# Kernel optimization log

Measured on AMD Instinct MI355X. Metric: run time of the kernel, lower is better.

The kernel has to match this reference:

```python
import jax, jax.numpy as jnp
import numpy as np

H = 8      # head count
ES = 96    # per-head dim
EMB = H * ES
L = 6      # layers
B, T = 8, 512
LN_EPS = 1e-5

def _layernorm(x, g, b):
    mu = jnp.mean(x, axis=-1, keepdims=True)
    var = jnp.mean(jnp.square(x - mu), axis=-1, keepdims=True)
    return (x - mu) * jax.lax.rsqrt(var + LN_EPS) * g + b

def setup_inputs() -> dict:
    key = jax.random.key(0)
    ks = jax.random.split(key, 6)
    s = 0.02
    return {
        "x": jax.random.normal(ks[0], (B, T, EMB), jnp.float32),
        "Wkqv": jax.random.normal(ks[1], (L, 3 * ES, ES), jnp.float32) * s,
        "Wproj": jax.random.normal(ks[2], (L, EMB, EMB), jnp.float32) * s,
        "ln1_g": jnp.ones((L, EMB), jnp.float32),
        "ln1_b": jnp.zeros((L, EMB), jnp.float32),
        "ln2_g": jnp.ones((L, EMB), jnp.float32),
        "ln2_b": jnp.zeros((L, EMB), jnp.float32),
        "ff_w1": jax.random.normal(ks[3], (L, 4 * EMB, EMB), jnp.float32) * s,
        "ff_b1": jnp.zeros((L, 4 * EMB), jnp.float32),
        "ff_w2": jax.random.normal(ks[4], (L, EMB, 4 * EMB), jnp.float32) * s,
        "ff_b2": jnp.zeros((L, EMB), jnp.float32),
    }

def _forward(x, Wkqv, Wproj, ln1_g, ln1_b, ln2_g, ln2_b, ff_w1, ff_b1, ff_w2, ff_b2):
    scale = 1.0 / jnp.sqrt(jnp.float32(ES))

    def step(carry, p):
        x, prev = carry
        wkqv, wproj, g1, b1, g2, b2, w1, bb1, w2, bb2 = p
        Bx, Tx, _ = x.shape
        xh = x.reshape(Bx, Tx, H, ES)                         # [B,T,H,es]
        kqv = jnp.einsum('bthe,fe->bthf', xh, wkqv)           # [B,T,H,3es]
        k, q, v = jnp.split(kqv, 3, axis=-1)                  # torch.split order: k,q,v
        # residual attention: raw scores + previous layer's raw scores
        score = jnp.einsum('bihk,bjhk->bijh', q, k) * scale + prev  # [B,T,T,H]
        att = jax.nn.softmax(score, axis=2)                   # over key axis j
        res = jnp.einsum('btih,bihs->bths', att, v).reshape(Bx, Tx, EMB)
        res = res @ wproj.T
        x = _layernorm(x + res, g1, b1)
        ff = jax.nn.gelu(x @ w1.T + bb1, approximate=False) @ w2.T + bb2
        x = _layernorm(x + ff, g2, b2)
        return (x, score), None

    prev0 = jnp.zeros((x.shape[0], x.shape[1], x.shape[1], H), x.dtype)
    (x, _), _ = jax.lax.scan(step, (x, prev0),
                             (Wkqv, Wproj, ln1_g, ln1_b, ln2_g, ln2_b,
                              ff_w1, ff_b1, ff_w2, ff_b2))
    return x

def reference(x, Wkqv, Wproj, ln1_g, ln1_b, ln2_g, ln2_b, ff_w1, ff_b1, ff_w2, ff_b2):
    return _forward(x, Wkqv, Wproj, ln1_g, ln1_b, ln2_g, ln2_b, ff_w1, ff_b1, ff_w2, ff_b2)
```

## Files before the change

### kernel.cpp

```cpp
#include <hip/hip_runtime.h>
#include <math.h>

#define BB 8
#define TT 512
#define HH 8
#define ESS 96
#define EMBD 768
#define FFD 3072
#define NLAYER 6
#define KHMAX 576

typedef unsigned short ushort_t;
typedef __attribute__((ext_vector_type(8))) short short8;
typedef __attribute__((ext_vector_type(4))) float f32x4;
typedef __attribute__((ext_vector_type(4))) unsigned short ushort4v;
typedef __attribute__((ext_vector_type(8))) unsigned short ushort8v;

static __device__ __forceinline__ ushort_t f2b(float f) {
    unsigned u = __builtin_bit_cast(unsigned, f);
    unsigned r = (u + 0x7fffu + ((u >> 16) & 1u)) >> 16;
    return (ushort_t)r;
}
static __device__ __forceinline__ float b2f(ushort_t u) {
    return __builtin_bit_cast(float, ((unsigned)u) << 16);
}

#define GLDS(gp, lp) __builtin_amdgcn_global_load_lds( \
    (const __attribute__((address_space(1))) void*)(gp), \
    (__attribute__((address_space(3))) void*)(lp), 16, 0, 0)

template<int BM, int BN, int WM, int WN, int OUTBF, int HASBIAS, int GELU, int BETA>
__global__ __launch_bounds__(256) void gemm_mfma(
    const ushort_t* __restrict__ A, int lda,
    const ushort_t* __restrict__ B, int ldb,
    void* __restrict__ Cv, int ldc,
    int K, float alpha,
    const float* __restrict__ bias,
    int bdiv, long sAb, long sAh, long sBb, long sBh, long sCb, long sCh)
{
    constexpr int BK = 32;
    constexpr int WTM = BM / WM;
    constexpr int WTN = BN / WN;
    constexpr int MF = WTM / 16, NF = WTN / 16;
    constexpr int ACH = (BM * BK * 2) / 1024;
    constexpr int BCH = (BN * BK * 2) / 1024;

    const int z = blockIdx.z;
    const int zb = z / bdiv, zh = z % bdiv;
    A += (long)zb * sAb + (long)zh * sAh;
    B += (long)zb * sBb + (long)zh * sBh;
    const long coff = (long)zb * sCb + (long)zh * sCh;

    __shared__ ushort_t As[BM * BK];
    __shared__ ushort_t Bs[BN * BK];

    const int tid = threadIdx.x;
    const int w = tid >> 6, lane = tid & 63;
    const int wr = w / WN, wc = w % WN;
    const int m0 = blockIdx.y * BM;
    const int n0 = blockIdx.x * BN;

    f32x4 acc[MF][NF] = {};

    const int fr = lane & 15;
    const int kb = lane >> 4;
    const int swz = ((fr >> 1) & 3) << 3;
    const int rl = lane >> 2;
    const int cl = ((lane & 3) * 8) ^ (((rl >> 1) & 3) << 3);

    for (int k0 = 0; k0 < K; k0 += BK) {
#pragma unroll
        for (int q = 0; q < (ACH + 3) / 4; ++q) {
            int ci = q * 4 + w;
            if (ci < ACH) {
                int r = ci * 16 + rl;
                GLDS(A + (long)(m0 + r) * lda + (k0 + cl), (char*)As + ci * 1024);
            }
        }
#pragma unroll
        for (int q = 0; q < (BCH + 3) / 4; ++q) {
            int ci = q * 4 + w;
            if (ci < BCH) {
                int r = ci * 16 + rl;
                GLDS(B + (long)(n0 + r) * ldb + (k0 + cl), (char*)Bs + ci * 1024);
            }
        }
        __syncthreads();

        short8 af[MF], bfr[NF];
#pragma unroll
        for (int fm = 0; fm < MF; ++fm)
            af[fm] = *(const short8*)&As[(wr * WTM + fm * 16 + fr) * 32 + (kb * 8 ^ swz)];
#pragma unroll
        for (int fn = 0; fn < NF; ++fn)
            bfr[fn] = *(const short8*)&Bs[(wc * WTN + fn * 16 + fr) * 32 + (kb * 8 ^ swz)];
#pragma unroll
        for (int fm = 0; fm < MF; ++fm)
#pragma unroll
            for (int fn = 0; fn < NF; ++fn)
                acc[fm][fn] = __builtin_amdgcn_mfma_f32_16x16x32_bf16(
                    af[fm], bfr[fn], acc[fm][fn], 0, 0, 0);
        __syncthreads();
    }

    const int cr = lane >> 4;
    const int cc = lane & 15;
#pragma unroll
    for (int fm = 0; fm < MF; ++fm) {
#pragma unroll
        for (int fn = 0; fn < NF; ++fn) {
#pragma unroll
            for (int j = 0; j < 4; ++j) {
                int gm = m0 + wr * WTM + fm * 16 + cr * 4 + j;
                int gn = n0 + wc * WTN + fn * 16 + cc;
                float v = alpha * acc[fm][fn][j];
                if (HASBIAS) v += bias[gn];
                if (GELU) {
                    float zz = 1.5957691216f * fmaf(0.044715f * v * v, v, v);
                    v = v / (1.f + __expf(-zz));
                }
                long idx = coff + (long)gm * ldc + gn;
                if (BETA) v += ((const float*)Cv)[idx];
                if (OUTBF) ((ushort_t*)Cv)[idx] = f2b(v);
                else       ((float*)Cv)[idx] = v;
            }
        }
    }
}

__global__ __launch_bounds__(256) void kqv_gemm(
    const ushort_t* __restrict__ A,
    const ushort_t* __restrict__ Bw,
    ushort_t* __restrict__ Kh, ushort_t* __restrict__ Qh,
    ushort_t* __restrict__ Vt, int loff, float scale)
{
    constexpr int BM = 128, BN = 96, BK = 32;
    __shared__ ushort_t As[BM * BK];
    __shared__ ushort_t Bs[BN * BK];

    const int tid = threadIdx.x;
    const int w = tid >> 6, lane = tid & 63;
    const int m0 = blockIdx.y * BM;
    const int n0 = blockIdx.x * BN;

    f32x4 acc[2][6] = {};
    const int fr = lane & 15;
    const int kb = lane >> 4;
    const int swz = ((fr >> 1) & 3) << 3;
    const int rl = lane >> 2;
    const int cl = ((lane & 3) * 8) ^ (((rl >> 1) & 3) << 3);

    for (int k0 = 0; k0 < 96; k0 += BK) {
#pragma unroll
        for (int q = 0; q < 2; ++q) {
            int ci = q * 4 + w;
            int r = ci * 16 + rl;
            GLDS(A + (long)(m0 + r) * ESS + (k0 + cl), (char*)As + ci * 1024);
        }
        {
            int ci = w;
            int r = ci * 16 + rl;
            GLDS(Bw + (long)(n0 + r) * ESS + (k0 + cl), (char*)Bs + ci * 1024);
            if (w < 2) {
                int ci2 = 4 + w;
                int r2 = ci2 * 16 + rl;
                GLDS(Bw + (long)(n0 + r2) * ESS + (k0 + cl), (char*)Bs + ci2 * 1024);
            }
        }
        __syncthreads();

        short8 af[2], bfr[6];
#pragma unroll
        for (int fm = 0; fm < 2; ++fm)
            af[fm] = *(const short8*)&As[(w * 32 + fm * 16 + fr) * 32 + (kb * 8 ^ swz)];
#pragma unroll
        for (int fn = 0; fn < 6; ++fn)
            bfr[fn] = *(const short8*)&Bs[(fn * 16 + fr) * 32 + (kb * 8 ^ swz)];
#pragma unroll
        for (int fm = 0; fm < 2; ++fm)
#pragma unroll
            for (int fn = 0; fn < 6; ++fn)
                acc[fm][fn] = __builtin_amdgcn_mfma_f32_16x16x32_bf16(
                    af[fm], bfr[fn], acc[fm][fn], 0, 0, 0);
        __syncthreads();
    }

    const int cr = lane >> 4;
    const int cc = lane & 15;
    const int kind = blockIdx.x;
#pragma unroll
    for (int fm = 0; fm < 2; ++fm) {
#pragma unroll
        for (int fn = 0; fn < 6; ++fn) {
#pragma unroll
            for (int j = 0; j < 4; ++j) {
                int gm = m0 + w * 32 + fm * 16 + cr * 4 + j;
                int s = fn * 16 + cc;
                float v = acc[fm][fn][j];
                int h = gm & 7;
                int bt = gm >> 3;
                int t = bt & 511, b = bt >> 9;
                int bh = b * HH + h;
                if (kind == 0)
                    Kh[((long)(bh * TT + t)) * KHMAX + loff + s] = f2b(v);
                else if (kind == 1)
                    Qh[((long)(bh * TT + t)) * KHMAX + loff + s] = f2b(v * scale);
                else
                    Vt[((long)(bh * ESS + s)) * TT + t] = f2b(v);
            }
        }
    }
}

__global__ __launch_bounds__(512) void fused_attn(
    const ushort_t* __restrict__ Qh,
    const ushort_t* __restrict__ Kh,
    const ushort_t* __restrict__ Vt,
    ushort_t* __restrict__ attn,
    int Kd)
{
    __shared__ char lds[79872];
    ushort_t* Pt  = (ushort_t*)lds;
    ushort_t* Bs  = (ushort_t*)lds;
    ushort_t* As  = (ushort_t*)(lds + 32768);
    ushort_t* Vs0 = (ushort_t*)(lds + 65536);
    ushort_t* Vs1 = (ushort_t*)(lds + 71680);
    float* red    = (float*)(lds + 77824);
    float* red2   = (float*)(lds + 78848);

    const int wg = blockIdx.x;
    const int xcd = wg & 7;
    const int sub = wg >> 3;
    const int m0 = (sub & 7) * 64;
    const int bh = (sub >> 3) * 8 + xcd;
    const int b = bh >> 3, h = bh & 7;

    const int tid = threadIdx.x;
    const int w = tid >> 6, lane = tid & 63;
    const int g = w >> 2;
    const int wg4 = w & 3;
    const int fr = lane & 15, kb = lane >> 4;
    const int cr = kb, cc = fr;
    const int swz = ((fr >> 1) & 3) << 3;

    const int rl = lane >> 2;
    const int cl = ((lane & 3) * 8) ^ (((rl >> 1) & 3) << 3);

    f32x4 acc[2][8] = {};

    for (int k0 = 0; k0 < Kd; k0 += 32) {
        if (w < 4) {
            int r = w * 16 + rl;
            GLDS(Qh + ((long)(bh * TT + m0 + r)) * KHMAX + k0 + cl,
                 (char*)As + w * 1024);
        }
#pragma unroll
        for (int q = 0; q < 4; ++q) {
            int ci = q * 8 + w;
            int r = ci * 16 + rl;
            GLDS(Kh + ((long)(bh * TT + r)) * KHMAX + k0 + cl,
                 (char*)Bs + ci * 1024);
        }
        __syncthreads();
        short8 af0 = *(const short8*)&As[(g * 32 + fr) * 32 + (kb * 8 ^ swz)];
        short8 af1 = *(const short8*)&As[(g * 32 + 16 + fr) * 32 + (kb * 8 ^ swz)];
#pragma unroll
        for (int fn = 0; fn < 8; ++fn) {
            short8 bf = *(const short8*)&Bs[(wg4 * 128 + fn * 16 + fr) * 32 + (kb * 8 ^ swz)];
            acc[0][fn] = __builtin_amdgcn_mfma_f32_16x16x32_bf16(af0, bf, acc[0][fn], 0, 0, 0);
            acc[1][fn] = __builtin_amdgcn_mfma_f32_16x16x32_bf16(af1, bf, acc[1][fn], 0, 0, 0);
        }
        __syncthreads();
    }

#pragma unroll
    for (int fm = 0; fm < 2; ++fm)
#pragma unroll
        for (int j = 0; j < 4; ++j) {
            float mx = -1e30f;
#pragma unroll
            for (int fn = 0; fn < 8; ++fn) mx = fmaxf(mx, acc[fm][fn][j]);
            for (int o = 1; o <= 8; o <<= 1) mx = fmaxf(mx, __shfl_xor(mx, o));
            if (cc == 0) red[g * 128 + wg4 * 32 + fm * 16 + cr * 4 + j] = mx;
        }
    __syncthreads();

    float inv[2][4];
#pragma unroll
    for (int fm = 0; fm < 2; ++fm)
#pragma unroll
        for (int j = 0; j < 4; ++j) {
            int r = fm * 16 + cr * 4 + j;
            const float* rg = red + g * 128;
            float mx = fmaxf(fmaxf(rg[r], rg[32 + r]), fmaxf(rg[64 + r], rg[96 + r]));
            float s = 0.f;
#pragma unroll
            for (int fn = 0; fn < 8; ++fn) {
                float e = __expf(acc[fm][fn][j] - mx);
                acc[fm][fn][j] = e;
                s += e;
            }
            for (int o = 1; o <= 8; o <<= 1) s += __shfl_xor(s, o);
            if (cc == 0) red2[g * 128 + wg4 * 32 + r] = s;
        }
    __syncthreads();
#pragma unroll
    for (int fm = 0; fm < 2; ++fm)
#pragma unroll
        for (int j = 0; j < 4; ++j) {
            int r = fm * 16 + cr * 4 + j;
            const float* rg = red2 + g * 128;
            inv[fm][j] = 1.f / (rg[r] + rg[32 + r] + rg[64 + r] + rg[96 + r]);
        }
    __syncthreads();

#pragma unroll
    for (int fm = 0; fm < 2; ++fm)
#pragma unroll
        for (int fn = 0; fn < 8; ++fn)
#pragma unroll
            for (int j = 0; j < 4; ++j) {
                int row = g * 32 + fm * 16 + cr * 4 + j;
                int col = wg4 * 128 + fn * 16 + cc;
                Pt[row * 512 + (col ^ ((row & 7) << 3))] = f2b(acc[fm][fn][j] * inv[fm][j]);
            }

    if (w < 6) {
        int r = w * 16 + rl;
        GLDS(Vt + ((long)(bh * ESS + r)) * TT + cl, (char*)Vs0 + w * 1024);
    }
    __syncthreads();

    const int wr = w >> 1, wc2 = w & 1;
    const int prow = wr * 16 + fr;
    f32x4 po[3] = {};
#pragma unroll
    for (int step = 0; step < 16; ++step) {
        const int j0 = step * 32;
        ushort_t* cur = (step & 1) ? Vs1 : Vs0;
        ushort_t* nxt = (step & 1) ? Vs0 : Vs1;
        if (step + 1 < 16 && w < 6) {
            int r = w * 16 + rl;
            GLDS(Vt + ((long)(bh * ESS + r)) * TT + j0 + 32 + cl, (char*)nxt + w * 1024);
        }
        short8 pa = *(const short8*)&Pt[prow * 512 + ((j0 + kb * 8) ^ ((prow & 7) << 3))];
#pragma unroll
        for (int fn = 0; fn < 3; ++fn) {
            short8 vb = *(const short8*)&cur[(wc2 * 48 + fn * 16 + fr) * 32 + (kb * 8 ^ swz)];
            po[fn] = __builtin_amdgcn_mfma_f32_16x16x32_bf16(pa, vb, po[fn], 0, 0, 0);
        }
        __syncthreads();
    }

#pragma unroll
    for (int fn = 0; fn < 3; ++fn)
#pragma unroll
        for (int j = 0; j < 4; ++j) {
            int grow = m0 + wr * 16 + cr * 4 + j;
            int gcol = h * ESS + wc2 * 48 + fn * 16 + cc;
            attn[((long)(b * TT + grow)) * EMBD + gcol] = f2b(po[fn][j]);
        }
}

__global__ __launch_bounds__(256) void cvt_f2b(
    const float* __restrict__ in, ushort_t* __restrict__ out)
{
    const int i = blockIdx.x * 256 + threadIdx.x;
    float4 v = ((const float4*)in)[i];
    ushort4v o = {f2b(v.x), f2b(v.y), f2b(v.z), f2b(v.w)};
    ((ushort4v*)out)[i] = o;
}

static __device__ __forceinline__ void cvt_w_one8(
    int r8, int layer,
    const float* Wkqv, const float* Wproj, const float* w1, const float* w2,
    ushort_t* dst_layer)
{
    const float* src; int base;
    if (r8 < 3456)        { src = Wkqv  + (long)layer * 27648;   base = 0; }
    else if (r8 < 77184)  { src = Wproj + (long)layer * 589824;  base = 3456; }
    else if (r8 < 372096) { src = w1    + (long)layer * 2359296; base = 77184; }
    else                  { src = w2    + (long)layer * 2359296; base = 372096; }
    int j = r8 - base;
    float4 v0 = ((const float4*)src)[j * 2];
    float4 v1 = ((const float4*)src)[j * 2 + 1];
    ushort8v o = {f2b(v0.x), f2b(v0.y), f2b(v0.z), f2b(v0.w),
                  f2b(v1.x), f2b(v1.y), f2b(v1.z), f2b(v1.w)};
    ((ushort8v*)dst_layer)[r8] = o;
}

__global__ __launch_bounds__(256) void cvt_weights_all(
    const float* __restrict__ Wkqv, const float* __restrict__ Wproj,
    const float* __restrict__ w1, const float* __restrict__ w2,
    ushort_t* __restrict__ dst)
{
    int i8 = blockIdx.x * 256 + threadIdx.x;
    int layer = i8 / 667008;
    int r8 = i8 - layer * 667008;
    cvt_w_one8(r8, layer, Wkqv, Wproj, w1, w2, dst + (long)layer * 5336064);
}

__global__ __launch_bounds__(256) void cvt_weights_layer(
    const float* __restrict__ Wkqv, const float* __restrict__ Wproj,
    const float* __restrict__ w1, const float* __restrict__ w2,
    ushort_t* __restrict__ dst, int layer)
{
    int r8 = blockIdx.x * 256 + threadIdx.x;
    cvt_w_one8(r8, layer, Wkqv, Wproj, w1, w2, dst);
}

template<int NR, int FINAL>
__global__ __launch_bounds__(192) void add_ln(
    ushort_t* __restrict__ xio, const ushort_t* __restrict__ res, long rstride,
    const float* __restrict__ bias,
    const float* __restrict__ g, const float* __restrict__ bta,
    float* __restrict__ xf)
{
    const long row = blockIdx.x;
    ushort4v* xr = (ushort4v*)(xio + row * EMBD);
    __shared__ float sh[4];
    const int tid = threadIdx.x;
    const int lane = tid & 63, w = tid >> 6;

    ushort4v xu = xr[tid];
    float v[4] = {b2f(xu.x), b2f(xu.y), b2f(xu.z), b2f(xu.w)};
#pragma unroll
    for (int p = 0; p < NR; ++p) {
        ushort4v u = ((const ushort4v*)(res + p * rstride + row * EMBD))[tid];
        v[0] += b2f(u.x); v[1] += b2f(u.y); v[2] += b2f(u.z); v[3] += b2f(u.w);
    }
    if (bias) {
        float4 b4 = ((const float4*)bias)[tid];
        v[0] += b4.x; v[1] += b4.y; v[2] += b4.z; v[3] += b4.w;
    }
    float s = v[0] + v[1] + v[2] + v[3];
    for (int o = 32; o; o >>= 1) s += __shfl_xor(s, o);
    if (lane == 0) sh[w] = s;
    __syncthreads();
    float mu = (sh[0] + sh[1] + sh[2]) * (1.f / EMBD);

    float var = 0.f;
#pragma unroll
    for (int c = 0; c < 4; ++c) { float d = v[c] - mu; var += d * d; }
    for (int o = 32; o; o >>= 1) var += __shfl_xor(var, o);
    __syncthreads();
    if (lane == 0) sh[w] = var;
    __syncthreads();
    var = (sh[0] + sh[1] + sh[2]) * (1.f / EMBD);
    float rstd = rsqrtf(var + 1e-5f);

    const float4 g4 = ((const float4*)g)[tid];
    const float4 b4 = ((const float4*)bta)[tid];
    float o0 = (v[0] - mu) * rstd * g4.x + b4.x;
    float o1 = (v[1] - mu) * rstd * g4.y + b4.y;
    float o2 = (v[2] - mu) * rstd * g4.z + b4.z;
    float o3 = (v[3] - mu) * rstd * g4.w + b4.w;
    ushort4v ob = {f2b(o0), f2b(o1), f2b(o2), f2b(o3)};
    xr[tid] = ob;
    if (FINAL) {
        float4 ov = {o0, o1, o2, o3};
        ((float4*)(xf + row * EMBD))[tid] = ov;
    }
}

extern "C" void kernel_launch(void* const* d_in, const int* in_sizes, int n_in,
                              void* d_out, int out_size, void* d_ws, size_t ws_size,
                              hipStream_t stream) {
    const float* x_in  = (const float*)d_in[0];
    const float* Wkqv  = (const float*)d_in[1];
    const float* Wproj = (const float*)d_in[2];
    const float* ln1_g = (const float*)d_in[3];
    const float* ln1_b = (const float*)d_in[4];
    const float* ln2_g = (const float*)d_in[5];
    const float* ln2_b = (const float*)d_in[6];
    const float* ff_w1 = (const float*)d_in[7];
    const float* ff_b1 = (const float*)d_in[8];
    const float* ff_w2 = (const float*)d_in[9];
    const float* ff_b2 = (const float*)d_in[10];

    float* xout = (float*)d_out;
    char* ws = (char*)d_ws;
    ushort_t* Qh     = (ushort_t*)(ws);
    ushort_t* Kh     = (ushort_t*)(ws + 37748736);
    ushort_t* Vtb    = (ushort_t*)(ws + 75497472);
    ushort_t* resb   = (ushort_t*)(ws + 75497472);
    ushort_t* h1b    = (ushort_t*)(ws + 100663296);
    ushort_t* xb     = (ushort_t*)(ws + 125829120);
    ushort_t* attnb  = (ushort_t*)(ws + 132120576);
    ushort_t* Wall   = (ushort_t*)(ws + 138412032);
    const size_t WLAYER_B = 10672128;
    const int    WLAYER_E = 5336064;
    const int big = (ws_size >= 138412032 + 6 * WLAYER_B) ? 1 : 0;
    const long RES_STRIDE = 3145728;

    cvt_f2b<<<3072, 256, 0, stream>>>(x_in, xb);
    if (big)
        cvt_weights_all<<<15633, 256, 0, stream>>>(Wkqv, Wproj, ff_w1, ff_w2, Wall);

    const float scale = 0.10206207261596577f;

    for (int l = 0; l < NLAYER; ++l) {
        const float* b1 = ff_b1 + (size_t)l * FFD;
        const float* b2 = ff_b2 + (size_t)l * EMBD;

        ushort_t* Wl = Wall + (big ? (long)l * WLAYER_E : 0);
        if (!big)
            cvt_weights_layer<<<2606, 256, 0, stream>>>(Wkqv, Wproj, ff_w1, ff_w2, Wl, l);
        ushort_t* Wkqvb  = Wl;
        ushort_t* Wprojb = Wl + 27648;
        ushort_t* W1b    = Wl + 617472;
        ushort_t* W2b    = Wl + 2976768;

        kqv_gemm<<<dim3(3, 256, 1), 256, 0, stream>>>(
            xb, Wkqvb, Kh, Qh, Vtb, l * ESS, scale);

        fused_attn<<<512, 512, 0, stream>>>(
            Qh, Kh, Vtb, attnb, ESS * (l + 1));

        gemm_mfma<128, 128, 2, 2, 1, 0, 0, 0><<<dim3(6, 32, 2), 256, 0, stream>>>(
            attnb, EMBD, Wprojb, EMBD, resb, EMBD, EMBD / 2, 1.f, nullptr,
            1, 384, 0, 384, 0, RES_STRIDE, 0);

        add_ln<2, 0><<<BB * TT, 192, 0, stream>>>(xb, resb, RES_STRIDE, nullptr,
            ln1_g + (size_t)l * EMBD, ln1_b + (size_t)l * EMBD, nullptr);

        gemm_mfma<128, 128, 2, 2, 1, 1, 1, 0><<<dim3(24, 32, 1), 256, 0, stream>>>(
            xb, EMBD, W1b, EMBD, h1b, FFD, EMBD, 1.f, b1,
            1, 0, 0, 0, 0, 0, 0);

        gemm_mfma<128, 128, 2, 2, 1, 0, 0, 0><<<dim3(6, 32, 4), 256, 0, stream>>>(
            h1b, FFD, W2b, FFD, resb, EMBD, FFD / 4, 1.f, nullptr,
            1, 768, 0, 768, 0, RES_STRIDE, 0);

        if (l == NLAYER - 1)
            add_ln<4, 1><<<BB * TT, 192, 0, stream>>>(xb, resb, RES_STRIDE, b2,
                ln2_g + (size_t)l * EMBD, ln2_b + (size_t)l * EMBD, xout);
        else
            add_ln<4, 0><<<BB * TT, 192, 0, stream>>>(xb, resb, RES_STRIDE, b2,
                ln2_g + (size_t)l * EMBD, ln2_b + (size_t)l * EMBD, nullptr);
    }
}
```

Before: 927.0 us.

## Split fused attention into QK-softmax kernel plus batched PV GEMM

Replaces the single fused attention kernel with two kernels when workspace allows: one computes QK scores over the concatenated residual K dimension and writes a normalized bf16 probability matrix to global memory, and a batched MFMA GEMM then multiplies the probabilities by V. This aims to lower LDS pressure and raise occupancy of the score kernel, and to reuse the tuned GEMM for the PV product. In exchange it adds a 32 MB round trip of the probability matrix through global memory plus an extra launch per layer. The fused path stays as a fallback when the workspace is too small.

```diff
diff --git a/kernel.cpp b/kernel.cpp
--- a/kernel.cpp
+++ b/kernel.cpp
@@ -212,12 +212,118 @@
     }
 }
 
-__global__ __launch_bounds__(512) void fused_attn(
+__global__ __launch_bounds__(512) void qk_softmax(
     const ushort_t* __restrict__ Qh,
     const ushort_t* __restrict__ Kh,
-    const ushort_t* __restrict__ Vt,
-    ushort_t* __restrict__ attn,
+    ushort_t* __restrict__ Pb,
     int Kd)
+{
+    __shared__ char lds[38912];
+    ushort_t* Bs = (ushort_t*)lds;
+    ushort_t* As = (ushort_t*)(lds + 32768);
+    float* red   = (float*)(lds + 36864);
+    float* red2  = (float*)(lds + 37888);
+
+    const int wg = blockIdx.x;
+    const int xcd = wg & 7;
+    const int sub = wg >> 3;
+    const int m0 = (sub & 7) * 64;
+    const int bh = (sub >> 3) * 8 + xcd;
+
+    const int tid = threadIdx.x;
+    const int w = tid >> 6, lane = tid & 63;
+    const int g = w >> 2;
+    const int wg4 = w & 3;
+    const int fr = lane & 15, kb = lane >> 4;
+    const int cr = kb, cc = fr;
+    const int swz = ((fr >> 1) & 3) << 3;
+
+    const int rl = lane >> 2;
+    const int cl = ((lane & 3) * 8) ^ (((rl >> 1) & 3) << 3);
+
+    f32x4 acc[2][8] = {};
+
+    for (int k0 = 0; k0 < Kd; k0 += 32) {
+        if (w < 4) {
+            int r = w * 16 + rl;
+            GLDS(Qh + ((long)(bh * TT + m0 + r)) * KHMAX + k0 + cl,
+                 (char*)As + w * 1024);
+        }
+#pragma unroll
+        for (int q = 0; q < 4; ++q) {
+            int ci = q * 8 + w;
+            int r = ci * 16 + rl;
+            GLDS(Kh + ((long)(bh * TT + r)) * KHMAX + k0 + cl,
+                 (char*)Bs + ci * 1024);
+        }
+        __syncthreads();
+        short8 af0 = *(const short8*)&As[(g * 32 + fr) * 32 + (kb * 8 ^ swz)];
+        short8 af1 = *(const short8*)&As[(g * 32 + 16 + fr) * 32 + (kb * 8 ^ swz)];
+#pragma unroll
+        for (int fn = 0; fn < 8; ++fn) {
+            short8 bf = *(const short8*)&Bs[(wg4 * 128 + fn * 16 + fr) * 32 + (kb * 8 ^ swz)];
+            acc[0][fn] = __builtin_amdgcn_mfma_f32_16x16x32_bf16(af0, bf, acc[0][fn], 0, 0, 0);
+            acc[1][fn] = __builtin_amdgcn_mfma_f32_16x16x32_bf16(af1, bf, acc[1][fn], 0, 0, 0);
+        }
+        __syncthreads();
+    }
+
+#pragma unroll
+    for (int fm = 0; fm < 2; ++fm)
+#pragma unroll
+        for (int j = 0; j < 4; ++j) {
+            float mx = -1e30f;
+#pragma unroll
+            for (int fn = 0; fn < 8; ++fn) mx = fmaxf(mx, acc[fm][fn][j]);
+            for (int o = 1; o <= 8; o <<= 1) mx = fmaxf(mx, __shfl_xor(mx, o));
+            if (cc == 0) red[g * 128 + wg4 * 32 + fm * 16 + cr * 4 + j] = mx;
+        }
+    __syncthreads();
+
+    float inv[2][4];
+#pragma unroll
+    for (int fm = 0; fm < 2; ++fm)
+#pragma unroll
+        for (int j = 0; j < 4; ++j) {
+            int r = fm * 16 + cr * 4 + j;
+            const float* rg = red + g * 128;
+            float mx = fmaxf(fmaxf(rg[r], rg[32 + r]), fmaxf(rg[64 + r], rg[96 + r]));
+            float s = 0.f;
+#pragma unroll
+            for (int fn = 0; fn < 8; ++fn) {
+                float e = __expf(acc[fm][fn][j] - mx);
+                acc[fm][fn][j] = e;
+                s += e;
+            }
+            for (int o = 1; o <= 8; o <<= 1) s += __shfl_xor(s, o);
+            if (cc == 0) red2[g * 128 + wg4 * 32 + r] = s;
+        }
+    __syncthreads();
+#pragma unroll
+    for (int fm = 0; fm < 2; ++fm)
+#pragma unroll
+        for (int j = 0; j < 4; ++j) {
+            int r = fm * 16 + cr * 4 + j;
+            const float* rg = red2 + g * 128;
+            inv[fm][j] = 1.f / (rg[r] + rg[32 + r] + rg[64 + r] + rg[96 + r]);
+        }
+
+    ushort_t* Prow = Pb + (long)bh * TT * TT;
+#pragma unroll
+    for (int fm = 0; fm < 2; ++fm)
+#pragma unroll
+        for (int fn = 0; fn < 8; ++fn)
+#pragma unroll
+            for (int j = 0; j < 4; ++j) {
+                int row = m0 + g * 32 + fm * 16 + cr * 4 + j;
+                int col = wg4 * 128 + fn * 16 + cc;
+                Prow[(long)row * TT + col] = f2b(acc[fm][fn][j] * inv[fm][j]);
+            }
+}
+
+__global__ __launch_bounds__(512) void fused_attn(
+    const ushort_t* __restrict__ Qh, const ushort_t* __restrict__ Kh,
+    const ushort_t* __restrict__ Vt, ushort_t* __restrict__ attn, int Kd)
 {
     __shared__ char lds[79872];
     ushort_t* Pt  = (ushort_t*)lds;
@@ -488,9 +594,11 @@
     ushort_t* xb     = (ushort_t*)(ws + 125829120);
     ushort_t* attnb  = (ushort_t*)(ws + 132120576);
     ushort_t* Wall   = (ushort_t*)(ws + 138412032);
+    ushort_t* Pb     = (ushort_t*)(ws + 202444800);
     const size_t WLAYER_B = 10672128;
     const int    WLAYER_E = 5336064;
-    const int big = (ws_size >= 138412032 + 6 * WLAYER_B) ? 1 : 0;
+    const int big  = (ws_size >= 202444800) ? 1 : 0;
+    const int big2 = (ws_size >= 202444800 + 33554432) ? 1 : 0;
     const long RES_STRIDE = 3145728;
 
     cvt_f2b<<<3072, 256, 0, stream>>>(x_in, xb);
@@ -514,8 +622,16 @@
         kqv_gemm<<<dim3(3, 256, 1), 256, 0, stream>>>(
             xb, Wkqvb, Kh, Qh, Vtb, l * ESS, scale);
 
-        fused_attn<<<512, 512, 0, stream>>>(
-            Qh, Kh, Vtb, attnb, ESS * (l + 1));
+        if (big2) {
+            qk_softmax<<<512, 512, 0, stream>>>(Qh, Kh, Pb, ESS * (l + 1));
+            gemm_mfma<64, 96, 2, 2, 1, 0, 0, 0><<<dim3(1, 8, BB * HH), 256, 0, stream>>>(
+                Pb, TT, Vtb, TT, attnb, EMBD, TT, 1.f, nullptr,
+                HH, (long)HH * TT * TT, (long)TT * TT,
+                (long)HH * ESS * TT, (long)ESS * TT,
+                (long)TT * EMBD, (long)ESS);
+        } else {
+            fused_attn<<<512, 512, 0, stream>>>(Qh, Kh, Vtb, attnb, ESS * (l + 1));
+        }
 
         gemm_mfma<128, 128, 2, 2, 1, 0, 0, 0><<<dim3(6, 32, 2), 256, 0, stream>>>(
             attnb, EMBD, Wprojb, EMBD, resb, EMBD, EMBD / 2, 1.f, nullptr,
```

Measured after the change: 1.001 ms. +8.0%, slower.
